# Kernel tuning notes

Measured on AMD Instinct MI355X. Metric: run time of the kernel, lower is better.

Reference implementation:

```python
import math
import jax, jax.numpy as jnp
import numpy as np

INV_SQRT_2_PI = math.pow(2.0 * math.pi, -0.5)

N_POINTS = 4_194_304
COMPONENTS = 128
MZ_MIN = 0.0
MZ_MAX = 1.0


def setup_inputs() -> dict:
    key = jax.random.key(0)
    k_mz, k_noise = jax.random.split(key)
    # evaluation points in the domain [mz_min, mz_max]
    mz = jax.random.uniform(k_mz, (N_POINTS,), dtype=jnp.float32,
                            minval=MZ_MIN, maxval=MZ_MAX)
    # parameter init mirrors GMM1D.__init__
    std_dev = 0.5 * (MZ_MAX - MZ_MIN) / COMPONENTS
    means = jnp.linspace(MZ_MIN, MZ_MAX, COMPONENTS, dtype=jnp.float32)
    noise = 0.5 * std_dev * jax.random.normal(k_noise, (COMPONENTS,), dtype=jnp.float32)
    mu = means + noise
    lv = jnp.full((COMPONENTS,), 2.0 * math.log(std_dev), dtype=jnp.float32)
    pi_l = jnp.zeros((COMPONENTS,), dtype=jnp.float32)
    return {"mz": mz, "pi_l": pi_l, "mu": mu, "lv": lv}


def reference(mz, pi_l, mu, lv):
    """GMM1D.prob: prob[n] = sum_k softmax(pi_l)_k * N(mz[n]; mu_k, exp(lv_k))"""
    pi = jax.nn.softmax(pi_l, axis=0)                      # [K]
    inv_var = jnp.exp(-lv)                                 # [K] = 1/sigma^2
    coef = pi * (INV_SQRT_2_PI * jnp.exp(-0.5 * lv))       # [K] pi_k / (sqrt(2pi) sigma_k)
    diff = mz[:, None] - mu[None, :]                       # [N, K]
    dens = jnp.exp(-0.5 * diff * diff * inv_var[None, :])  # [N, K] unnormalized gaussian
    prob = jnp.einsum('nk,k->n', dens, coef)               # [N]
    return prob
```

## Files before the change

### kernel.cpp

```cpp
#include <hip/hip_runtime.h>
#include <math.h>

#define K_COMP 128
#define LOG2E 1.4426950408889634f
#define INV_SQRT_2PI 0.3989422804014327f
#define PPT 16
#define BLOCK 256
#define REP 32


template <int W, int OFF>
__device__ __forceinline__ void eval_mu_only(const float* __restrict__ smu,
                                             int lrep, float A, float scale,
                                             const float* x, float* acc) {
    #pragma unroll
    for (int p = 0; p < PPT; p++) {
        float xp = x[p];
        int k0 = min(max((int)(xp * 127.0f) - OFF, 0), K_COMP - W);
        const float* mrow = &smu[(k0 << 5) + lrep];
        float mv[W];
        #pragma unroll
        for (int j = 0; j < W; j++)
            mv[j] = mrow[j << 5];
        float a0 = 0.0f, a1 = 0.0f;
        #pragma unroll
        for (int j = 0; j < W; j += 2) {
            float d0 = xp - mv[j];
            a0 += __builtin_amdgcn_exp2f(d0 * A * d0);
            float d1 = xp - mv[j + 1];
            a1 += __builtin_amdgcn_exp2f(d1 * A * d1);
        }
        acc[p] = (a0 + a1) * scale;
    }
}

template <int W, int OFF>
__device__ __forceinline__ void eval_window(const float* __restrict__ smu,
                                            const float* __restrict__ slc,
                                            int lrep, float A,
                                            const float* x, float* acc) {
    #pragma unroll
    for (int p = 0; p < PPT; p++) {
        float xp = x[p];
        int k0 = min(max((int)(xp * 127.0f) - OFF, 0), K_COMP - W);
        const float* mrow = &smu[(k0 << 5) + lrep];
        const float* crow = &slc[(k0 << 5) + lrep];
        float mv[W], cv[W];
        #pragma unroll
        for (int j = 0; j < W; j++) {
            mv[j] = mrow[j << 5];
            cv[j] = crow[j << 5];
        }
        float a0 = 0.0f, a1 = 0.0f;
        #pragma unroll
        for (int j = 0; j < W; j += 2) {
            float d0 = xp - mv[j];
            a0 += __builtin_amdgcn_exp2f(__builtin_fmaf(d0 * A, d0, cv[j]));
            float d1 = xp - mv[j + 1];
            a1 += __builtin_amdgcn_exp2f(__builtin_fmaf(d1 * A, d1, cv[j + 1]));
        }
        acc[p] = a0 + a1;
    }
}

__global__ __launch_bounds__(BLOCK) void gmm_fused(const float* __restrict__ mz,
                                                   const float* __restrict__ pi_l,
                                                   const float* __restrict__ mu,
                                                   const float* __restrict__ lv,
                                                   float* __restrict__ out,
                                                   int n) {
    __shared__ float smu[K_COMP * REP];
    __shared__ float slc[K_COMP * REP];
    __shared__ float4 sRaw[K_COMP];
    __shared__ float sAs, sScale;
    __shared__ int sWin;

    int tid = threadIdx.x;

    if (tid < 64) {
        int t = tid;
        float p0 = pi_l[t];
        float p1 = pi_l[t + 64];
        float m = fmaxf(p0, p1);
        #pragma unroll
        for (int off = 1; off < 64; off <<= 1)
            m = fmaxf(m, __shfl_xor(m, off, 64));
        float e0 = expf(p0 - m);
        float e1 = expf(p1 - m);
        float s = e0 + e1;
        #pragma unroll
        for (int off = 1; off < 64; off <<= 1)
            s += __shfl_xor(s, off, 64);
        float inv_s = 1.0f / s;

        float r12 = 0.0f, r30 = 0.0f;
        float amin = 1e30f, amax = -1e30f;
        float lmin = 1e30f, lmax = -1e30f;
        #pragma unroll
        for (int j = 0; j < 2; j++) {
            int k = t + 64 * j;
            float e = (j == 0) ? e0 : e1;
            float pi_k = e * inv_s;
            float lvk = lv[k];
            float A = -0.5f * expf(-lvk) * LOG2E;
            float coef = pi_k * INV_SQRT_2PI * expf(-0.5f * lvk);
            float lc = log2f(coef);
            float muk = mu[k];
            sRaw[k] = make_float4(muk, A, lc, 0.0f);
            float del = fabsf(muk * 127.0f - (float)k);
            float d12 = sqrtf(fmaxf(lc + 12.0f, 0.0f) / (-A)) * 127.0f;
            float d30 = sqrtf(fmaxf(lc + 30.0f, 0.0f) / (-A)) * 127.0f;
            r12 = fmaxf(r12, del + d12);
            r30 = fmaxf(r30, del + d30);
            amin = fminf(amin, A);  amax = fmaxf(amax, A);
            lmin = fminf(lmin, lc); lmax = fmaxf(lmax, lc);
        }
        #pragma unroll
        for (int off = 1; off < 64; off <<= 1) {
            r12 = fmaxf(r12, __shfl_xor(r12, off, 64));
            r30 = fmaxf(r30, __shfl_xor(r30, off, 64));
            amin = fminf(amin, __shfl_xor(amin, off, 64));
            amax = fmaxf(amax, __shfl_xor(amax, off, 64));
            lmin = fminf(lmin, __shfl_xor(lmin, off, 64));
            lmax = fmaxf(lmax, __shfl_xor(lmax, off, 64));
        }
        if (t == 0) {
            sAs = amax;
            sScale = __builtin_amdgcn_exp2f(lmax);
            int w = 0;
            if (amin == amax) {
                if (r12 <= 3.0f)      w = (lmin == lmax) ? 3 : 2;
                else if (r30 <= 5.0f) w = 1;
            }
            sWin = w;
        }
    }
    __syncthreads();

    const int win = sWin;

    {
        int r = tid & 31;
        int kb = (tid >> 5) << 4;
        if (win == 3) {
            #pragma unroll
            for (int i = 0; i < 16; i++) {
                int k = kb + i;
                smu[(k << 5) + r] = sRaw[k].x;
            }
        } else {
            #pragma unroll
            for (int i = 0; i < 16; i++) {
                int k = kb + i;
                float4 raw = sRaw[k];
                smu[(k << 5) + r] = raw.x;
                slc[(k << 5) + r] = raw.z;
            }
        }
    }
    __syncthreads();

    const float A = sAs;
    const float scale = sScale;
    const int lrep = tid & (REP - 1);
    long blockBase = (long)blockIdx.x * (BLOCK * PPT);

    const float4* mz4 = (const float4*)mz;
    long base4 = blockBase >> 2;
    float x[PPT];
    #pragma unroll
    for (int g = 0; g < PPT / 4; g++) {
        float4 v = mz4[base4 + (long)g * BLOCK + tid];
        x[g * 4 + 0] = v.x; x[g * 4 + 1] = v.y;
        x[g * 4 + 2] = v.z; x[g * 4 + 3] = v.w;
    }

    float acc[PPT];
    if (win == 3) {
        eval_mu_only<8, 3>(smu, lrep, A, scale, x, acc);
    } else if (win == 2) {
        eval_window<8, 3>(smu, slc, lrep, A, x, acc);
    } else if (win == 1) {
        eval_window<12, 5>(smu, slc, lrep, A, x, acc);
    } else {
        #pragma unroll
        for (int p = 0; p < PPT; p++) acc[p] = 0.0f;
        for (int k = 0; k < K_COMP; k++) {
            float4 raw = sRaw[k];
            #pragma unroll
            for (int p = 0; p < PPT; p++) {
                float d = x[p] - raw.x;
                float t = __builtin_fmaf(d * raw.y, d, raw.z);
                acc[p] += __builtin_amdgcn_exp2f(t);
            }
        }
    }

    float4* out4 = (float4*)out;
    #pragma unroll
    for (int g = 0; g < PPT / 4; g++) {
        float4 v = make_float4(acc[g * 4 + 0], acc[g * 4 + 1],
                               acc[g * 4 + 2], acc[g * 4 + 3]);
        out4[base4 + (long)g * BLOCK + tid] = v;
    }
}

extern "C" void kernel_launch(void* const* d_in, const int* in_sizes, int n_in,
                              void* d_out, int out_size, void* d_ws, size_t ws_size,
                              hipStream_t stream) {
    const float* mz   = (const float*)d_in[0];
    const float* pi_l = (const float*)d_in[1];
    const float* mu   = (const float*)d_in[2];
    const float* lv   = (const float*)d_in[3];
    float* out = (float*)d_out;
    int n = in_sizes[0];

    int grid = (n + BLOCK * PPT - 1) / (BLOCK * PPT);
    gmm_fused<<<grid, BLOCK, 0, stream>>>(mz, pi_l, mu, lv, out, n);
}
```

Before: 78.96 us.

## Prefetch inputs before parameter setup, pre-scale means, halve points per thread

```diff
diff --git a/kernel.cpp b/kernel.cpp
--- a/kernel.cpp
+++ b/kernel.cpp
@@ -4,78 +4,67 @@
 #define K_COMP 128
 #define LOG2E 1.4426950408889634f
 #define INV_SQRT_2PI 0.3989422804014327f
-#define PPT 16
+#define PPT 8
 #define BLOCK 256
 #define REP 32
 
 
-template <int W, int OFF>
-__device__ __forceinline__ void eval_mu_only(const float* __restrict__ smu,
-                                             int lrep, float A, float scale,
-                                             const float* x, float* acc) {
+template <int W, int OFF, bool UNIF_LC>
+__device__ __forceinline__ void eval_win(const float* __restrict__ smu,
+                                         const float* __restrict__ lcz,
+                                         int lrep, float sscl, float lc_u,
+                                         const float* x, float* acc) {
     #pragma unroll
     for (int p = 0; p < PPT; p++) {
         float xp = x[p];
         int k0 = min(max((int)(xp * 127.0f) - OFF, 0), K_COMP - W);
         const float* mrow = &smu[(k0 << 5) + lrep];
-        float mv[W];
-        #pragma unroll
-        for (int j = 0; j < W; j++)
-            mv[j] = mrow[j << 5];
+        float sx = xp * sscl;
         float a0 = 0.0f, a1 = 0.0f;
-        #pragma unroll
-        for (int j = 0; j < W; j += 2) {
-            float d0 = xp - mv[j];
-            a0 += __builtin_amdgcn_exp2f(d0 * A * d0);
-            float d1 = xp - mv[j + 1];
-            a1 += __builtin_amdgcn_exp2f(d1 * A * d1);
-        }
-        acc[p] = (a0 + a1) * scale;
-    }
-}
-
-template <int W, int OFF>
-__device__ __forceinline__ void eval_window(const float* __restrict__ smu,
-                                            const float* __restrict__ slc,
-                                            int lrep, float A,
-                                            const float* x, float* acc) {
-    #pragma unroll
-    for (int p = 0; p < PPT; p++) {
-        float xp = x[p];
-        int k0 = min(max((int)(xp * 127.0f) - OFF, 0), K_COMP - W);
-        const float* mrow = &smu[(k0 << 5) + lrep];
-        const float* crow = &slc[(k0 << 5) + lrep];
-        float mv[W], cv[W];
-        #pragma unroll
-        for (int j = 0; j < W; j++) {
-            mv[j] = mrow[j << 5];
-            cv[j] = crow[j << 5];
-        }
-        float a0 = 0.0f, a1 = 0.0f;
-        #pragma unroll
-        for (int j = 0; j < W; j += 2) {
-            float d0 = xp - mv[j];
-            a0 += __builtin_amdgcn_exp2f(__builtin_fmaf(d0 * A, d0, cv[j]));
-            float d1 = xp - mv[j + 1];
-            a1 += __builtin_amdgcn_exp2f(__builtin_fmaf(d1 * A, d1, cv[j + 1]));
+        if (UNIF_LC) {
+            float mv[W];
+            #pragma unroll
+            for (int j = 0; j < W; j++)
+                mv[j] = mrow[j << 5];
+            #pragma unroll
+            for (int j = 0; j < W; j += 2) {
+                float sd0 = sx - mv[j];
+                a0 += __builtin_amdgcn_exp2f(__builtin_fmaf(sd0, -sd0, lc_u));
+                float sd1 = sx - mv[j + 1];
+                a1 += __builtin_amdgcn_exp2f(__builtin_fmaf(sd1, -sd1, lc_u));
+            }
+        } else {
+            const float* crow = lcz + ((long)k0 << 2);
+            #pragma unroll
+            for (int j = 0; j < W; j++) {
+                float mvj = mrow[j << 5];
+                float lcj = crow[j << 2];
+                float sd = sx - mvj;
+                float e = __builtin_amdgcn_exp2f(__builtin_fmaf(sd, -sd, lcj));
+                if (j & 1) a1 += e; else a0 += e;
+            }
         }
         acc[p] = a0 + a1;
     }
 }
 
-__global__ __launch_bounds__(BLOCK) void gmm_fused(const float* __restrict__ mz,
-                                                   const float* __restrict__ pi_l,
-                                                   const float* __restrict__ mu,
-                                                   const float* __restrict__ lv,
-                                                   float* __restrict__ out,
-                                                   int n) {
+__global__ __launch_bounds__(BLOCK, 8) void gmm_fused(const float* __restrict__ mz,
+                                                      const float* __restrict__ pi_l,
+                                                      const float* __restrict__ mu,
+                                                      const float* __restrict__ lv,
+                                                      float* __restrict__ out,
+                                                      int n) {
     __shared__ float smu[K_COMP * REP];
-    __shared__ float slc[K_COMP * REP];
     __shared__ float4 sRaw[K_COMP];
-    __shared__ float sAs, sScale;
+    __shared__ float sLC, sS;
     __shared__ int sWin;
 
     int tid = threadIdx.x;
+
+    const float4* mz4 = (const float4*)mz;
+    long base4 = (long)blockIdx.x * (BLOCK * PPT / 4) + tid;
+    float4 v0 = mz4[base4];
+    float4 v1 = mz4[base4 + BLOCK];
 
     if (tid < 64) {
         int t = tid;
@@ -93,28 +82,23 @@
             s += __shfl_xor(s, off, 64);
         float inv_s = 1.0f / s;
 
-        float r12 = 0.0f, r30 = 0.0f;
-        float amin = 1e30f, amax = -1e30f;
-        float lmin = 1e30f, lmax = -1e30f;
-        #pragma unroll
-        for (int j = 0; j < 2; j++) {
-            int k = t + 64 * j;
-            float e = (j == 0) ? e0 : e1;
-            float pi_k = e * inv_s;
-            float lvk = lv[k];
-            float A = -0.5f * expf(-lvk) * LOG2E;
-            float coef = pi_k * INV_SQRT_2PI * expf(-0.5f * lvk);
-            float lc = log2f(coef);
-            float muk = mu[k];
-            sRaw[k] = make_float4(muk, A, lc, 0.0f);
-            float del = fabsf(muk * 127.0f - (float)k);
-            float d12 = sqrtf(fmaxf(lc + 12.0f, 0.0f) / (-A)) * 127.0f;
-            float d30 = sqrtf(fmaxf(lc + 30.0f, 0.0f) / (-A)) * 127.0f;
-            r12 = fmaxf(r12, del + d12);
-            r30 = fmaxf(r30, del + d30);
-            amin = fminf(amin, A);  amax = fmaxf(amax, A);
-            lmin = fminf(lmin, lc); lmax = fmaxf(lmax, lc);
-        }
+        float lv0 = lv[t],      lv1 = lv[t + 64];
+        float mu0 = mu[t],      mu1 = mu[t + 64];
+        float A0 = -0.5f * expf(-lv0) * LOG2E;
+        float A1 = -0.5f * expf(-lv1) * LOG2E;
+        float lc0 = log2f(e0 * inv_s * INV_SQRT_2PI * expf(-0.5f * lv0));
+        float lc1 = log2f(e1 * inv_s * INV_SQRT_2PI * expf(-0.5f * lv1));
+
+        float del0 = fabsf(mu0 * 127.0f - (float)t);
+        float del1 = fabsf(mu1 * 127.0f - (float)(t + 64));
+        float d12_0 = sqrtf(fmaxf(lc0 + 12.0f, 0.0f) / (-A0)) * 127.0f;
+        float d12_1 = sqrtf(fmaxf(lc1 + 12.0f, 0.0f) / (-A1)) * 127.0f;
+        float d30_0 = sqrtf(fmaxf(lc0 + 30.0f, 0.0f) / (-A0)) * 127.0f;
+        float d30_1 = sqrtf(fmaxf(lc1 + 30.0f, 0.0f) / (-A1)) * 127.0f;
+        float r12 = fmaxf(del0 + d12_0, del1 + d12_1);
+        float r30 = fmaxf(del0 + d30_0, del1 + d30_1);
+        float amin = fminf(A0, A1),  amax = fmaxf(A0, A1);
+        float lmin = fminf(lc0, lc1), lmax = fmaxf(lc0, lc1);
         #pragma unroll
         for (int off = 1; off < 64; off <<= 1) {
             r12 = fmaxf(r12, __shfl_xor(r12, off, 64));
@@ -124,9 +108,12 @@
             lmin = fminf(lmin, __shfl_xor(lmin, off, 64));
             lmax = fmaxf(lmax, __shfl_xor(lmax, off, 64));
         }
+        float sscl = sqrtf(-amax);
+        sRaw[t]      = make_float4(mu0 * sscl, A0, lc0, mu0);
+        sRaw[t + 64] = make_float4(mu1 * sscl, A1, lc1, mu1);
         if (t == 0) {
-            sAs = amax;
-            sScale = __builtin_amdgcn_exp2f(lmax);
+            sS = sscl;
+            sLC = lmax;
             int w = 0;
             if (amin == amax) {
                 if (r12 <= 3.0f)      w = (lmin == lmax) ? 3 : 2;
@@ -139,57 +126,42 @@
 
     const int win = sWin;
 
-    {
+    if (win) {
         int r = tid & 31;
         int kb = (tid >> 5) << 4;
-        if (win == 3) {
-            #pragma unroll
-            for (int i = 0; i < 16; i++) {
-                int k = kb + i;
-                smu[(k << 5) + r] = sRaw[k].x;
-            }
-        } else {
-            #pragma unroll
-            for (int i = 0; i < 16; i++) {
-                int k = kb + i;
-                float4 raw = sRaw[k];
-                smu[(k << 5) + r] = raw.x;
-                slc[(k << 5) + r] = raw.z;
-            }
+        #pragma unroll
+        for (int i = 0; i < 16; i++) {
+            int k = kb + i;
+            smu[(k << 5) + r] = sRaw[k].x;
         }
     }
     __syncthreads();
 
-    const float A = sAs;
-    const float scale = sScale;
+    float x[PPT];
+    x[0] = v0.x; x[1] = v0.y; x[2] = v0.z; x[3] = v0.w;
+    x[4] = v1.x; x[5] = v1.y; x[6] = v1.z; x[7] = v1.w;
+
+    const float sscl = sS;
+    const float lcu = sLC;
     const int lrep = tid & (REP - 1);
-    long blockBase = (long)blockIdx.x * (BLOCK * PPT);
-
-    const float4* mz4 = (const float4*)mz;
-    long base4 = blockBase >> 2;
-    float x[PPT];
-    #pragma unroll
-    for (int g = 0; g < PPT / 4; g++) {
-        float4 v = mz4[base4 + (long)g * BLOCK + tid];
-        x[g * 4 + 0] = v.x; x[g * 4 + 1] = v.y;
-        x[g * 4 + 2] = v.z; x[g * 4 + 3] = v.w;
-    }
+    const float* lcz = ((const float*)sRaw) + 2;
 
     float acc[PPT];
     if (win == 3) {
-        eval_mu_only<8, 3>(smu, lrep, A, scale, x, acc);
+        eval_win<8, 3, true>(smu, lcz, lrep, sscl, lcu, x, acc);
     } else if (win == 2) {
-        eval_window<8, 3>(smu, slc, lrep, A, x, acc);
+        eval_win<8, 3, false>(smu, lcz, lrep, sscl, 0.0f, x, acc);
     } else if (win == 1) {
-        eval_window<12, 5>(smu, slc, lrep, A, x, acc);
+        eval_win<12, 5, false>(smu, lcz, lrep, sscl, 0.0f, x, acc);
     } else {
         #pragma unroll
         for (int p = 0; p < PPT; p++) acc[p] = 0.0f;
+        #pragma unroll 2
         for (int k = 0; k < K_COMP; k++) {
             float4 raw = sRaw[k];
             #pragma unroll
             for (int p = 0; p < PPT; p++) {
-                float d = x[p] - raw.x;
+                float d = x[p] - raw.w;
                 float t = __builtin_fmaf(d * raw.y, d, raw.z);
                 acc[p] += __builtin_amdgcn_exp2f(t);
             }
@@ -197,12 +169,8 @@
     }
 
     float4* out4 = (float4*)out;
-    #pragma unroll
-    for (int g = 0; g < PPT / 4; g++) {
-        float4 v = make_float4(acc[g * 4 + 0], acc[g * 4 + 1],
-                               acc[g * 4 + 2], acc[g * 4 + 3]);
-        out4[base4 + (long)g * BLOCK + tid] = v;
-    }
+    out4[base4] = make_float4(acc[0], acc[1], acc[2], acc[3]);
+    out4[base4 + BLOCK] = make_float4(acc[4], acc[5], acc[6], acc[7]);
 }
 
 extern "C" void kernel_launch(void* const* d_in, const int* in_sizes, int n_in,
```

Result: no change. 79.45 us (+0.6%).
